# Optimization experiments

Hardware: AMD Instinct MI355X
Metric: run time of the kernel (lower is better)

## Reference

```python
import jax, jax.numpy as jnp
import numpy as np

HID = 1024

def setup_inputs() -> dict:
    key = jax.random.key(0)
    k1, k2, k3, k4, k5 = jax.random.split(key, 5)
    B, S, H = 16, 2048, HID
    queries = jax.random.normal(k1, (B, H), dtype=jnp.float32)
    keys = jax.random.normal(k2, (B, S, H), dtype=jnp.float32)
    values = jax.random.normal(k3, (B, S, H), dtype=jnp.float32)
    # additive_attention params: Linear(2H->H), ReLU, Linear(H->1)
    s1 = 1.0 / np.sqrt(2 * H)
    s2 = 1.0 / np.sqrt(H)
    W1 = jax.random.uniform(k4, (2 * H, H), dtype=jnp.float32, minval=-s1, maxval=s1)
    b1 = jnp.zeros((H,), dtype=jnp.float32)
    W2 = jax.random.uniform(k5, (H, 1), dtype=jnp.float32, minval=-s2, maxval=s2)
    b2 = jnp.zeros((1,), dtype=jnp.float32)
    return {"queries": queries, "keys": keys, "values": values,
            "W1": W1, "b1": b1, "W2": W2, "b2": b2}

def reference(queries, keys, values, W1, b1, W2, b2):
    B, S, H = keys.shape
    # concat expanded query with keys along feature dim: [B,S,2H]
    q_exp = jnp.broadcast_to(queries[:, None, :], (B, S, H))
    concat = jnp.concatenate([q_exp, keys], axis=-1)
    h = jax.nn.relu(jnp.einsum('bsf,fh->bsh', concat, W1) + b1)
    scores = jnp.einsum('bsh,ho->bso', h, W2) + b2          # [B,S,1]
    alphas = jax.nn.softmax(scores, axis=1)                  # softmax over seq
    # context = alphas^T @ values : [B,1,H]
    context = jnp.einsum('bso,bsh->boh', alphas, values)
    return (context, alphas)
```

## Files before the change

### kernel.cpp

```cpp
#include <hip/hip_runtime.h>

#define HID 1024
#define SEQ 2048
#define NB  16

typedef __attribute__((ext_vector_type(8))) short bf16x8;
typedef __attribute__((ext_vector_type(4))) float f32x4;

static __device__ __forceinline__ short f2bf(float f) {
    union { float f; unsigned u; } v; v.f = f;
    unsigned u = v.u + 0x7fffu + ((v.u >> 16) & 1u);
    return (short)(u >> 16);
}
static __device__ __forceinline__ unsigned pk2(float a, float b) {
    return (unsigned)(unsigned short)f2bf(a) | ((unsigned)(unsigned short)f2bf(b) << 16);
}
static __device__ __forceinline__ void glds16(const void* g, void* l) {
    __builtin_amdgcn_global_load_lds(
        (const __attribute__((address_space(1))) unsigned*)g,
        (__attribute__((address_space(3))) unsigned*)l, 16, 0, 0);
}

__global__ __launch_bounds__(256) void prep_all(const float* __restrict__ keys,
                                                short* __restrict__ kbf,
                                                const float* __restrict__ W1,
                                                const float* __restrict__ queries,
                                                const float* __restrict__ b1,
                                                short* __restrict__ w1t,
                                                float* __restrict__ qproj,
                                                int nconv) {
    __shared__ float shmem[2048];
    const int tid = threadIdx.x;
    int bw = blockIdx.x;

    if (bw < 32) {
        const int f0 = (bw >> 2) * 128;
        const int n0 = (bw & 3) * 256;
#pragma unroll
        for (int j = 0; j < 8; ++j) {
            const int idx = tid * 8 + j;
            const int b = idx >> 7, f = idx & 127;
            shmem[idx] = queries[b * HID + f0 + f];
        }
        __syncthreads();
        float acc[16];
        const float bv = (bw >> 2 == 0) ? b1[n0 + tid] : 0.0f;
#pragma unroll
        for (int b = 0; b < 16; ++b) acc[b] = (b == 0) ? bv : 0.0f;
        if (bw >> 2 == 0) {
#pragma unroll
            for (int b = 1; b < 16; ++b) acc[b] = bv;
        }
        for (int f = 0; f < 128; ++f) {
            const float w = W1[(size_t)(f0 + f) * HID + n0 + tid];
#pragma unroll
            for (int b = 0; b < 16; ++b)
                acc[b] += shmem[b * 128 + f] * w;
        }
#pragma unroll
        for (int b = 0; b < 16; ++b)
            atomicAdd(&qproj[b * HID + n0 + tid], acc[b]);
        return;
    }
    bw -= 32;
    if (bw < 1024) {
        float (*t)[33] = (float(*)[33])shmem;
        const int k0 = (bw & 31) * 32;
        const int n0 = (bw >> 5) * 32;
        const int tx = tid & 31, ty = tid >> 5;
#pragma unroll
        for (int i = 0; i < 32; i += 8)
            t[ty + i][tx] = W1[(size_t)(HID + k0 + ty + i) * HID + n0 + tx];
        __syncthreads();
#pragma unroll
        for (int i = 0; i < 32; i += 8)
            w1t[(size_t)(n0 + ty + i) * HID + k0 + tx] = f2bf(t[tx][ty + i]);
        return;
    }
    bw -= 1024;
    if (bw < nconv) {
        const size_t i = ((size_t)bw * 256 + tid) * 8;
        const float4 a = *(const float4*)(keys + i);
        const float4 b = *(const float4*)(keys + i + 4);
        int4 o;
        o.x = (int)pk2(a.x, a.y); o.y = (int)pk2(a.z, a.w);
        o.z = (int)pk2(b.x, b.y); o.w = (int)pk2(b.z, b.w);
        *(int4*)(kbf + i) = o;
    }
}

template<int PRE>
__global__ __launch_bounds__(256) void score_gemm128(const float* __restrict__ keys,
                                                     const short* __restrict__ kbf,
                                                     const short* __restrict__ w1t,
                                                     const float* __restrict__ qproj,
                                                     const float* __restrict__ W2,
                                                     float* __restrict__ scores) {
    __shared__ short As[128 * 32];
    __shared__ short Bs[128 * 32];

    const int tid  = threadIdx.x;
    const int lane = tid & 63;
    const int wave = tid >> 6;
    const int n0 = blockIdx.x * 128;
    const int m0 = blockIdx.y * 128;
    const int batch = m0 >> 11;
    const int wm = wave >> 1, wn = wave & 1;
    const int q = lane >> 4, c = lane & 15;

    const int lrow = lane >> 2;
    const int lk   = (lane & 3) * 8;

    f32x4 acc[4][4] = {};

    for (int k0 = 0; k0 < HID; k0 += 32) {
#pragma unroll
        for (int call = 0; call < 2; ++call) {
            const int rbase = (wave * 2 + call) * 16;
            glds16(w1t + (size_t)(n0 + rbase + lrow) * HID + k0 + lk,
                   &Bs[rbase * 32]);
        }
        if (PRE) {
#pragma unroll
            for (int call = 0; call < 2; ++call) {
                const int rbase = (wave * 2 + call) * 16;
                glds16(kbf + (size_t)(m0 + rbase + lrow) * HID + k0 + lk,
                       &As[rbase * 32]);
            }
        } else {
            const int r = tid >> 1, h = (tid & 1) * 16;
            const float* src = keys + (size_t)(m0 + r) * HID + k0 + h;
            const float4 v0 = *(const float4*)(src + 0);
            const float4 v1 = *(const float4*)(src + 4);
            const float4 v2 = *(const float4*)(src + 8);
            const float4 v3 = *(const float4*)(src + 12);
            int4 o0, o1;
            o0.x = (int)pk2(v0.x, v0.y); o0.y = (int)pk2(v0.z, v0.w);
            o0.z = (int)pk2(v1.x, v1.y); o0.w = (int)pk2(v1.z, v1.w);
            o1.x = (int)pk2(v2.x, v2.y); o1.y = (int)pk2(v2.z, v2.w);
            o1.z = (int)pk2(v3.x, v3.y); o1.w = (int)pk2(v3.z, v3.w);
            *(int4*)&As[r * 32 + h + 0] = o0;
            *(int4*)&As[r * 32 + h + 8] = o1;
        }
        __syncthreads();

        bf16x8 af[4], bf[4];
#pragma unroll
        for (int i = 0; i < 4; ++i)
            af[i] = *(const bf16x8*)&As[(wm * 64 + i * 16 + c) * 32 + q * 8];
#pragma unroll
        for (int i = 0; i < 4; ++i)
            bf[i] = *(const bf16x8*)&Bs[(wn * 64 + i * 16 + c) * 32 + q * 8];
#pragma unroll
        for (int mi = 0; mi < 4; ++mi)
#pragma unroll
            for (int ni = 0; ni < 4; ++ni)
                acc[mi][ni] = __builtin_amdgcn_mfma_f32_16x16x32_bf16(af[mi], bf[ni], acc[mi][ni], 0, 0, 0);
        __syncthreads();
    }

    const float* qp = qproj + batch * HID + n0 + wn * 64;
    const float* w2 = W2 + n0 + wn * 64;
    float psum[4][4] = {};
#pragma unroll
    for (int ni = 0; ni < 4; ++ni) {
        const float qv = qp[ni * 16 + c];
        const float wv = w2[ni * 16 + c];
#pragma unroll
        for (int mi = 0; mi < 4; ++mi)
#pragma unroll
            for (int r = 0; r < 4; ++r)
                psum[mi][r] += fmaxf(acc[mi][ni][r] + qv, 0.f) * wv;
    }
#pragma unroll
    for (int m = 1; m < 16; m <<= 1)
#pragma unroll
        for (int mi = 0; mi < 4; ++mi)
#pragma unroll
            for (int r = 0; r < 4; ++r)
                psum[mi][r] += __shfl_xor(psum[mi][r], m, 64);
    if (c == 0) {
#pragma unroll
        for (int mi = 0; mi < 4; ++mi) {
            const int row = m0 + wm * 64 + mi * 16 + q * 4;
#pragma unroll
            for (int r = 0; r < 4; ++r)
                atomicAdd(&scores[row + r], psum[mi][r]);
        }
    }
}

__global__ __launch_bounds__(256) void softmax_k(const float* __restrict__ scores,
                                                 float* __restrict__ alphas,
                                                 float* __restrict__ ctx) {
    __shared__ float red[256];
    const int b = blockIdx.x;
    const int tid = threadIdx.x;
    float4 z = {0.f, 0.f, 0.f, 0.f};
    *(float4*)(ctx + b * HID + tid * 4) = z;

    float loc[8];
    float mx = -1e30f;
#pragma unroll
    for (int i = 0; i < 8; ++i) {
        loc[i] = scores[b * SEQ + tid + i * 256];
        mx = fmaxf(mx, loc[i]);
    }
    red[tid] = mx; __syncthreads();
    for (int s = 128; s > 0; s >>= 1) {
        if (tid < s) red[tid] = fmaxf(red[tid], red[tid + s]);
        __syncthreads();
    }
    mx = red[0]; __syncthreads();
    float sum = 0.f;
#pragma unroll
    for (int i = 0; i < 8; ++i) { loc[i] = expf(loc[i] - mx); sum += loc[i]; }
    red[tid] = sum; __syncthreads();
    for (int s = 128; s > 0; s >>= 1) {
        if (tid < s) red[tid] += red[tid + s];
        __syncthreads();
    }
    const float inv = 1.0f / red[0];
#pragma unroll
    for (int i = 0; i < 8; ++i) alphas[b * SEQ + tid + i * 256] = loc[i] * inv;
}

__global__ __launch_bounds__(256) void context_k(const float* __restrict__ alphas,
                                                 const float* __restrict__ values,
                                                 float* __restrict__ context) {
    const int b = blockIdx.y;
    const int s0 = blockIdx.x * 64;
    const int col = threadIdx.x * 4;
    float4 acc = {0.f, 0.f, 0.f, 0.f};
    for (int i = 0; i < 64; ++i) {
        const int s = s0 + i;
        const float a = alphas[b * SEQ + s];
        const float4 v = *(const float4*)(values + (size_t)(b * SEQ + s) * HID + col);
        acc.x += a * v.x; acc.y += a * v.y; acc.z += a * v.z; acc.w += a * v.w;
    }
    float* cp = context + b * HID + col;
    atomicAdd(cp + 0, acc.x);
    atomicAdd(cp + 1, acc.y);
    atomicAdd(cp + 2, acc.z);
    atomicAdd(cp + 3, acc.w);
}

extern "C" void kernel_launch(void* const* d_in, const int* in_sizes, int n_in,
                              void* d_out, int out_size, void* d_ws, size_t ws_size,
                              hipStream_t stream) {
    const float* queries = (const float*)d_in[0];
    const float* keys    = (const float*)d_in[1];
    const float* values  = (const float*)d_in[2];
    const float* W1      = (const float*)d_in[3];
    const float* b1      = (const float*)d_in[4];
    const float* W2      = (const float*)d_in[5];

    float* out_ctx   = (float*)d_out;
    float* out_alpha = (float*)d_out + NB * HID;

    char* ws = (char*)d_ws;
    float* scores = (float*)ws;
    float* qproj  = (float*)(ws + 131072);
    short* w1t    = (short*)(ws + 196608);
    short* kbf    = (short*)(ws + 2293760);

    const size_t need_pre = 2293760ull + 67108864ull;
    const bool pre = ws_size >= need_pre;
    const int nconv = pre ? 16384 : 0;

    hipMemsetAsync(ws, 0, 196608, stream);

    prep_all<<<32 + 1024 + nconv, 256, 0, stream>>>(
        keys, kbf, W1, queries, b1, w1t, qproj, nconv);

    if (pre)
        score_gemm128<1><<<dim3(8, 256), 256, 0, stream>>>(keys, kbf, w1t, qproj, W2, scores);
    else
        score_gemm128<0><<<dim3(8, 256), 256, 0, stream>>>(keys, kbf, w1t, qproj, W2, scores);

    softmax_k<<<NB, 256, 0, stream>>>(scores, out_alpha, out_ctx);
    context_k<<<dim3(32, NB), 256, 0, stream>>>(out_alpha, values, out_ctx);
}
```

Measured before the change: 383.0 us.

## Fuse softmax with context, fold memset into prep, swizzle GEMM blocks

Replaces the workspace memset with zeroing blocks inside the prep kernel and computes the query projection in four blocks without atomics. Remaps score GEMM block indices so neighbouring blocks share weight tiles for better cache reuse. Fuses softmax and context into one kernel where each block recomputes the softmax into shared memory, removing a launch and the alpha reload. The trade-off is redundant softmax work and a longer serial query-projection loop in a few blocks.

```diff
diff --git a/kernel.cpp b/kernel.cpp
--- a/kernel.cpp
+++ b/kernel.cpp
@@ -28,41 +28,51 @@
                                                 const float* __restrict__ b1,
                                                 short* __restrict__ w1t,
                                                 float* __restrict__ qproj,
+                                                float* __restrict__ scores,
+                                                float* __restrict__ ctx,
                                                 int nconv) {
     __shared__ float shmem[2048];
     const int tid = threadIdx.x;
     int bw = blockIdx.x;
 
+    if (bw < 4) {
+        const int n = bw * 256 + tid;
+        float acc[16];
+#pragma unroll
+        for (int b = 0; b < 16; ++b) acc[b] = b1[n];
+        for (int f0 = 0; f0 < HID; f0 += 128) {
+#pragma unroll
+            for (int j = 0; j < 8; ++j) {
+                const int idx = tid * 8 + j;
+                shmem[idx] = queries[(idx >> 7) * HID + f0 + (idx & 127)];
+            }
+            __syncthreads();
+#pragma unroll 4
+            for (int f = 0; f < 128; ++f) {
+                const float w = W1[(size_t)(f0 + f) * HID + n];
+#pragma unroll
+                for (int b = 0; b < 16; ++b)
+                    acc[b] += shmem[b * 128 + f] * w;
+            }
+            __syncthreads();
+        }
+#pragma unroll
+        for (int b = 0; b < 16; ++b) qproj[b * HID + n] = acc[b];
+        return;
+    }
+    bw -= 4;
     if (bw < 32) {
-        const int f0 = (bw >> 2) * 128;
-        const int n0 = (bw & 3) * 256;
-#pragma unroll
-        for (int j = 0; j < 8; ++j) {
-            const int idx = tid * 8 + j;
-            const int b = idx >> 7, f = idx & 127;
-            shmem[idx] = queries[b * HID + f0 + f];
-        }
-        __syncthreads();
-        float acc[16];
-        const float bv = (bw >> 2 == 0) ? b1[n0 + tid] : 0.0f;
-#pragma unroll
-        for (int b = 0; b < 16; ++b) acc[b] = (b == 0) ? bv : 0.0f;
-        if (bw >> 2 == 0) {
-#pragma unroll
-            for (int b = 1; b < 16; ++b) acc[b] = bv;
-        }
-        for (int f = 0; f < 128; ++f) {
-            const float w = W1[(size_t)(f0 + f) * HID + n0 + tid];
-#pragma unroll
-            for (int b = 0; b < 16; ++b)
-                acc[b] += shmem[b * 128 + f] * w;
-        }
-#pragma unroll
-        for (int b = 0; b < 16; ++b)
-            atomicAdd(&qproj[b * HID + n0 + tid], acc[b]);
+        float4 z = {0.f, 0.f, 0.f, 0.f};
+        *(float4*)(scores + (size_t)(bw * 256 + tid) * 4) = z;
         return;
     }
     bw -= 32;
+    if (bw < 16) {
+        float4 z = {0.f, 0.f, 0.f, 0.f};
+        *(float4*)(ctx + (size_t)(bw * 256 + tid) * 4) = z;
+        return;
+    }
+    bw -= 16;
     if (bw < 1024) {
         float (*t)[33] = (float(*)[33])shmem;
         const int k0 = (bw & 31) * 32;
@@ -102,9 +112,14 @@
     const int tid  = threadIdx.x;
     const int lane = tid & 63;
     const int wave = tid >> 6;
-    const int n0 = blockIdx.x * 128;
-    const int m0 = blockIdx.y * 128;
-    const int batch = m0 >> 11;
+
+    const int b     = blockIdx.x + blockIdx.y * 8;
+    const int n_idx = (b >> 3) & 7;
+    const int m_idx = ((b >> 6) << 3) | (b & 7);
+    const int n0 = n_idx * 128;
+    const int m0 = m_idx * 128;
+    const int batch = m_idx >> 4;
+
     const int wm = wave >> 1, wn = wave & 1;
     const int q = lane >> 4, c = lane & 15;
 
@@ -190,14 +205,15 @@
     }
 }
 
-__global__ __launch_bounds__(256) void softmax_k(const float* __restrict__ scores,
-                                                 float* __restrict__ alphas,
-                                                 float* __restrict__ ctx) {
+__global__ __launch_bounds__(256) void softmax_context(const float* __restrict__ scores,
+                                                       const float* __restrict__ values,
+                                                       float* __restrict__ alphas,
+                                                       float* __restrict__ ctx) {
     __shared__ float red[256];
-    const int b = blockIdx.x;
+    __shared__ float ash[SEQ];
+    const int b = blockIdx.y;
+    const int x = blockIdx.x;
     const int tid = threadIdx.x;
-    float4 z = {0.f, 0.f, 0.f, 0.f};
-    *(float4*)(ctx + b * HID + tid * 4) = z;
 
     float loc[8];
     float mx = -1e30f;
@@ -222,27 +238,28 @@
     }
     const float inv = 1.0f / red[0];
 #pragma unroll
-    for (int i = 0; i < 8; ++i) alphas[b * SEQ + tid + i * 256] = loc[i] * inv;
-}
-
-__global__ __launch_bounds__(256) void context_k(const float* __restrict__ alphas,
-                                                 const float* __restrict__ values,
-                                                 float* __restrict__ context) {
-    const int b = blockIdx.y;
-    const int s0 = blockIdx.x * 64;
-    const int col = threadIdx.x * 4;
-    float4 acc = {0.f, 0.f, 0.f, 0.f};
+    for (int i = 0; i < 8; ++i) ash[tid + i * 256] = loc[i] * inv;
+    __syncthreads();
+
+    if (x == 32) {
+#pragma unroll
+        for (int i = 0; i < 8; ++i)
+            alphas[b * SEQ + tid + i * 256] = loc[i] * inv;
+        return;
+    }
+    const int s0 = x * 64;
+    const int col = tid * 4;
+    float4 acc4 = {0.f, 0.f, 0.f, 0.f};
     for (int i = 0; i < 64; ++i) {
-        const int s = s0 + i;
-        const float a = alphas[b * SEQ + s];
-        const float4 v = *(const float4*)(values + (size_t)(b * SEQ + s) * HID + col);
-        acc.x += a * v.x; acc.y += a * v.y; acc.z += a * v.z; acc.w += a * v.w;
-    }
-    float* cp = context + b * HID + col;
-    atomicAdd(cp + 0, acc.x);
-    atomicAdd(cp + 1, acc.y);
-    atomicAdd(cp + 2, acc.z);
-    atomicAdd(cp + 3, acc.w);
+        const float a = ash[s0 + i];
+        const float4 v = *(const float4*)(values + (size_t)(b * SEQ + s0 + i) * HID + col);
+        acc4.x += a * v.x; acc4.y += a * v.y; acc4.z += a * v.z; acc4.w += a * v.w;
+    }
+    float* cp = ctx + b * HID + col;
+    atomicAdd(cp + 0, acc4.x);
+    atomicAdd(cp + 1, acc4.y);
+    atomicAdd(cp + 2, acc4.z);
+    atomicAdd(cp + 3, acc4.w);
 }
 
 extern "C" void kernel_launch(void* const* d_in, const int* in_sizes, int n_in,
@@ -268,16 +285,13 @@
     const bool pre = ws_size >= need_pre;
     const int nconv = pre ? 16384 : 0;
 
-    hipMemsetAsync(ws, 0, 196608, stream);
-
-    prep_all<<<32 + 1024 + nconv, 256, 0, stream>>>(
-        keys, kbf, W1, queries, b1, w1t, qproj, nconv);
+    prep_all<<<4 + 32 + 16 + 1024 + nconv, 256, 0, stream>>>(
+        keys, kbf, W1, queries, b1, w1t, qproj, scores, out_ctx, nconv);
 
     if (pre)
         score_gemm128<1><<<dim3(8, 256), 256, 0, stream>>>(keys, kbf, w1t, qproj, W2, scores);
     else
         score_gemm128<0><<<dim3(8, 256), 256, 0, stream>>>(keys, kbf, w1t, qproj, W2, scores);
 
-    softmax_k<<<NB, 256, 0, stream>>>(scores, out_alpha, out_ctx);
-    context_k<<<dim3(32, NB), 256, 0, stream>>>(out_alpha, values, out_ctx);
-}
+    softmax_context<<<dim3(33, NB), 256, 0, stream>>>(scores, values, out_alpha, out_ctx);
+}
```

Measured after the change: 514.0 us. 1.34x slower.
